# Kernel tuning notes

Measured on AMD Instinct MI355X. Metric: run time of the kernel, lower is better.

The kernel has to match this reference:

```python
import jax, jax.numpy as jnp
import numpy as np
import math

D_MODEL = 1024
N_HEAD = 16          # sub-heads per branch
N_BR = 4             # hardcoded n_branches
DH = D_MODEL // N_HEAD
H_TOT = N_BR * N_HEAD
B, T = 1, 1024
SCALE = math.pi / math.sqrt(3.0)
ATTNSCALE = DH ** -0.5


def _rope(x):
    # x: [B, H, T, D]; matches torch RoPE: even/odd split, concat halves
    t_len, d = x.shape[2], x.shape[-1]
    inv_freq = 1.0 / (10000.0 ** (jnp.arange(0, d, 2, dtype=jnp.float32) / d))
    freqs = jnp.arange(t_len, dtype=jnp.float32)[:, None] * inv_freq[None, :]  # [T, D/2]
    cos, sin = jnp.cos(freqs), jnp.sin(freqs)
    x1, x2 = x[..., 0::2], x[..., 1::2]
    return jnp.concatenate([-x2 * sin + x1 * cos, x1 * sin + x2 * cos], axis=-1)


def setup_inputs() -> dict:
    key = jax.random.key(0)
    ks = jax.random.split(key, 12)
    s = D_MODEL ** -0.5
    return {
        "X": jax.random.normal(ks[0], (B, T, D_MODEL), jnp.float32),
        "W_Q": jax.random.normal(ks[1], (D_MODEL, D_MODEL * N_BR), jnp.float32) * s,
        "b_Q": jax.random.normal(ks[2], (D_MODEL * N_BR,), jnp.float32) * 0.02,
        "W_K": jax.random.normal(ks[3], (D_MODEL, D_MODEL), jnp.float32) * s,
        "b_K": jax.random.normal(ks[4], (D_MODEL,), jnp.float32) * 0.02,
        "W_V": jax.random.normal(ks[5], (D_MODEL, D_MODEL), jnp.float32) * s,
        "b_V": jax.random.normal(ks[6], (D_MODEL,), jnp.float32) * 0.02,
        "sink_scalars": jax.random.uniform(ks[7], (H_TOT,), jnp.float32, 0.0, 0.1),
        "v_nulls": jax.random.normal(ks[8], (N_BR, D_MODEL), jnp.float32) * 0.02,
        "W_O": jax.random.normal(ks[9], (N_BR, D_MODEL, D_MODEL), jnp.float32) * s,
        "W_O_bias": jax.random.normal(ks[10], (N_BR, D_MODEL), jnp.float32) * 0.02,
    }


def reference(X, W_Q, b_Q, W_K, b_K, W_V, b_V, sink_scalars, v_nulls, W_O, W_O_bias):
    Bv, Tv, C = X.shape
    # projections -> [B, H, T, Dh]
    q = (X @ W_Q + b_Q).reshape(Bv, Tv, H_TOT, DH).transpose(0, 2, 1, 3)
    k_base = (X @ W_K + b_K).reshape(Bv, Tv, N_HEAD, DH).transpose(0, 2, 1, 3)
    v_base = (X @ W_V + b_V).reshape(Bv, Tv, N_HEAD, DH).transpose(0, 2, 1, 3)
    k = jnp.tile(k_base, (1, N_BR, 1, 1))
    v = jnp.tile(v_base, (1, N_BR, 1, 1))
    q, k = _rope(q), _rope(k)

    scores = jnp.einsum("bhtd,bhsd->bhts", q, k) * ATTNSCALE
    key_self = jnp.clip(jnp.sum(k * k, axis=-1), 1e-6, None)      # [B,H,S]
    w = jax.nn.softplus(scores / jnp.sqrt(key_self)[:, :, None, :])
    causal = jnp.tril(jnp.ones((Tv, Tv), bool))                    # [T,S]
    w = jnp.where(causal, w, 0.0)
    w = w * jax.nn.sigmoid(SCALE * w)
    sinks = sink_scalars.reshape(1, H_TOT, 1, 1)
    w = jnp.where(w < sinks, 0.0, w)
    # concat-with-sink renormalization, expressed without the concat
    total = jnp.sum(w, axis=-1, keepdims=True) + sinks + 1e-6      # [B,H,T,1]
    probs_tokens = w / total
    probs_sink = sinks / total                                     # [B,H,T,1]

    out = jnp.einsum("bhts,bhsd->bhtd", probs_tokens, v)
    v_null = v_nulls.reshape(H_TOT, DH)[None, :, None, :]          # [1,H,1,Dh]
    out = out + probs_sink * v_null

    context = out.reshape(Bv, N_BR, N_HEAD, Tv, DH).transpose(0, 1, 3, 2, 4)
    context = context.reshape(Bv, N_BR, Tv, C)
    y = jnp.einsum("bntc,ncd->bntd", context, W_O) + W_O_bias[None, :, None, :]
    return y.mean(axis=1)
```

## Files before the change

### kernel.cpp

```cpp
#include <hip/hip_runtime.h>
#include <math.h>

typedef __attribute__((ext_vector_type(4))) float  f32x4;
typedef __attribute__((ext_vector_type(8))) short  bf16x8;
typedef __attribute__((ext_vector_type(4))) short  s16x4;

#define SQUISH_U 1.8137993642342178f
#define LN2F     0.69314718055994531f

__device__ __forceinline__ float b2f(short u) {
    union { float f; unsigned b; } v; v.b = ((unsigned)(unsigned short)u) << 16; return v.f;
}
__device__ __forceinline__ short f2b(float f) {
    union { float f; unsigned b; } v; v.f = f;
    unsigned r = (v.b + 0x7FFFu + ((v.b >> 16) & 1u)) >> 16;
    return (short)r;
}
__device__ __forceinline__ unsigned cvt_pk_bf16(float lo, float hi) {
    unsigned r;
    asm("v_cvt_pk_bf16_f32 %0, %1, %2" : "=v"(r) : "v"(lo), "v"(hi));
    return r;
}
__device__ __forceinline__ void gll16(const void* g, void* l) {
    __builtin_amdgcn_global_load_lds((const __attribute__((address_space(1))) void*)g,
                                     (__attribute__((address_space(3))) void*)l, 16, 0, 0);
}
__device__ __forceinline__ void gll4(const void* g, void* l) {
    __builtin_amdgcn_global_load_lds((const __attribute__((address_space(1))) void*)g,
                                     (__attribute__((address_space(3))) void*)l, 4, 0, 0);
}

__device__ __forceinline__ void do_transpose(const float* __restrict__ src, int R, int C,
                                             short* __restrict__ dst, float scale,
                                             int c0, int r0, float (*tile)[65], int tid) {
    #pragma unroll
    for (int it = 0; it < 4; ++it) {
        int lin = it * 256 + tid;
        int r = lin >> 4, c4 = lin & 15;
        f32x4 v = *(const f32x4*)(src + (size_t)(r0 + r) * C + c0 + c4 * 4);
        #pragma unroll
        for (int k = 0; k < 4; ++k) tile[r][c4 * 4 + k] = v[k];
    }
    __syncthreads();
    #pragma unroll
    for (int it = 0; it < 4; ++it) {
        int lin = it * 256 + tid;
        int c = lin >> 4, rq = lin & 15;
        s16x4 o;
        #pragma unroll
        for (int k = 0; k < 4; ++k) o[k] = f2b(tile[rq * 4 + k][c] * scale);
        *(s16x4*)(dst + (size_t)(c0 + c) * R + r0 + rq * 4) = o;
    }
}

__global__ __launch_bounds__(256) void prep_kernel(
    const float* __restrict__ X, const float* __restrict__ W_Q, const float* __restrict__ W_K,
    const float* __restrict__ W_V, const float* __restrict__ W_O,
    const float* __restrict__ bQ, const float* __restrict__ bK, const float* __restrict__ bV,
    const float* __restrict__ bO,
    short* __restrict__ Xb, short* __restrict__ WbT, short* __restrict__ WoT,
    float* __restrict__ biasQKV, float* __restrict__ out) {
    __shared__ float tile[64][65];
    const int bid = blockIdx.x, tid = threadIdx.x;
    if (bid < 256) {
        int i = (bid * 256 + tid) * 16;
        #pragma unroll
        for (int k = 0; k < 4; ++k) {
            f32x4 v = *(const f32x4*)(X + i + k * 4);
            s16x4 o;
            o.x = f2b(v.x); o.y = f2b(v.y); o.z = f2b(v.z); o.w = f2b(v.w);
            *(s16x4*)(Xb + i + k * 4) = o;
        }
    } else if (bid < 1280) {
        int b2 = bid - 256;
        do_transpose(W_Q, 1024, 4096, WbT, 1.f, (b2 & 63) * 64, (b2 >> 6) * 64, tile, tid);
    } else if (bid < 1536) {
        int b2 = bid - 1280;
        do_transpose(W_K, 1024, 1024, WbT + 4096 * 1024, 1.f, (b2 & 15) * 64, (b2 >> 4) * 64, tile, tid);
    } else if (bid < 1792) {
        int b2 = bid - 1536;
        do_transpose(W_V, 1024, 1024, WbT + 5120 * 1024, 1.f, (b2 & 15) * 64, (b2 >> 4) * 64, tile, tid);
    } else if (bid < 2816) {
        int b2 = bid - 1792;
        do_transpose(W_O, 4096, 1024, WoT, 0.25f, (b2 & 15) * 64, (b2 >> 4) * 64, tile, tid);
    } else if (bid < 2840) {
        int i = (bid - 2816) * 256 + tid;
        if (i < 4096)      biasQKV[i] = bQ[i];
        else if (i < 5120) biasQKV[i] = bK[i - 4096];
        else               biasQKV[i] = bV[i - 5120];
    } else {
        int i = ((bid - 2840) * 256 + tid) * 4;
        f32x4 v;
        #pragma unroll
        for (int k = 0; k < 4; ++k) {
            int c = (i + k) & 1023;
            v[k] = 0.25f * (bO[c] + bO[1024 + c] + bO[2048 + c] + bO[3072 + c]);
        }
        *(f32x4*)(out + i) = v;
    }
}

#define GSTAGE_64x128(k0_, b_) do {                                            \
    _Pragma("unroll")                                                          \
    for (int it = 0; it < 2; ++it) {                                           \
        int lin0 = it * 256 + wave * 64;                                       \
        int lin = lin0 + lane;                                                 \
        int r = lin >> 3, c = (lin & 7) ^ (r & 7);                             \
        gll16(A + (size_t)(m0 + r) * K + (k0_) + c * 8, (char*)lA[b_] + lin0 * 16); \
    }                                                                          \
    _Pragma("unroll")                                                          \
    for (int it = 0; it < 4; ++it) {                                           \
        int lin0 = it * 256 + wave * 64;                                       \
        int lin = lin0 + lane;                                                 \
        int r = lin >> 3, c = (lin & 7) ^ (r & 7);                             \
        gll16(BT + (size_t)(n0 + r) * K + (k0_) + c * 8, (char*)lB[b_] + lin0 * 16); \
    } } while (0)

#define GEMM_CORE_64x128(kbeg_, kend_)                                         \
    GSTAGE_64x128(kbeg_, 0);                                                   \
    int cur = 0;                                                               \
    for (int k0 = (kbeg_); k0 < (kend_); k0 += 64) {                           \
        if (k0 + 64 < (kend_)) {                                               \
            GSTAGE_64x128(k0 + 64, cur ^ 1);                                   \
            asm volatile("s_waitcnt vmcnt(6) lgkmcnt(0)" ::: "memory");        \
        } else {                                                               \
            asm volatile("s_waitcnt vmcnt(0) lgkmcnt(0)" ::: "memory");        \
        }                                                                      \
        __builtin_amdgcn_s_barrier();                                          \
        _Pragma("unroll")                                                      \
        for (int kk = 0; kk < 2; ++kk) {                                       \
            bf16x8 af[2], bf_[4];                                              \
            _Pragma("unroll")                                                  \
            for (int m = 0; m < 2; ++m) {                                      \
                int row = wr * 32 + m * 16 + l15;                              \
                int ch = (kk * 4 + l4) ^ (row & 7);                            \
                af[m] = *(const bf16x8*)&lA[cur][row][ch << 3];                \
            }                                                                  \
            _Pragma("unroll")                                                  \
            for (int n = 0; n < 4; ++n) {                                      \
                int row = wc * 64 + n * 16 + l15;                              \
                int ch = (kk * 4 + l4) ^ (row & 7);                            \
                bf_[n] = *(const bf16x8*)&lB[cur][row][ch << 3];               \
            }                                                                  \
            _Pragma("unroll")                                                  \
            for (int m = 0; m < 2; ++m)                                        \
                _Pragma("unroll")                                              \
                for (int n = 0; n < 4; ++n)                                    \
                    acc[m][n] = __builtin_amdgcn_mfma_f32_16x16x32_bf16(af[m], bf_[n], acc[m][n], 0, 0, 0); \
        }                                                                      \
        asm volatile("" ::: "memory");                                         \
        __builtin_amdgcn_s_barrier();                                          \
        cur ^= 1;                                                              \
    }

__global__ __launch_bounds__(256, 3) void gemm_qkvf_kernel(
    const short* __restrict__ A, const short* __restrict__ BT,
    const float* __restrict__ bias, short* __restrict__ QKVb,
    short* __restrict__ Vtb, float* __restrict__ ksr,
    int M, int N, int K) {
    __shared__ short lA[2][64][64];
    __shared__ short lB[2][128][64];
    const int tid = threadIdx.x;
    const int lane = tid & 63, wave = tid >> 6;
    const int l15 = lane & 15, l4 = lane >> 4;
    const int wr = wave >> 1, wc = wave & 1;
    const int n0 = blockIdx.x * 128, m0 = blockIdx.y * 64;

    f32x4 acc[2][4];
    const f32x4 fz = {0.f, 0.f, 0.f, 0.f};
    #pragma unroll
    for (int m = 0; m < 2; ++m)
        #pragma unroll
        for (int n = 0; n < 4; ++n) acc[m][n] = fz;

    GEMM_CORE_64x128(0, K);

    const int head = blockIdx.x * 2 + wc;
    float bn[4];
    #pragma unroll
    for (int n = 0; n < 4; ++n) bn[n] = bias[head * 64 + n * 16 + l15];
    #pragma unroll
    for (int m = 0; m < 2; ++m)
        #pragma unroll
        for (int n = 0; n < 4; ++n)
            #pragma unroll
            for (int r = 0; r < 4; ++r) acc[m][n][r] += bn[n];

    if (head < 80) {
        const float invf0 = __builtin_exp2f(-(float)l15 * 0.41524101186092033f);
        const float invf1 = invf0 * 0.01f;
        const int p1 = (2 * l15) & 15, p2 = (2 * l15 + 1) & 15;
        #pragma unroll
        for (int m = 0; m < 2; ++m) {
            int tb = m0 + wr * 32 + m * 16 + l4 * 4;
            float x1lo[4], x2lo[4], x1hi[4], x2hi[4];
            #pragma unroll
            for (int r = 0; r < 4; ++r) {
                float a0 = __shfl(acc[m][0][r], p1, 16), b0 = __shfl(acc[m][1][r], p1, 16);
                float a1 = __shfl(acc[m][0][r], p2, 16), b1 = __shfl(acc[m][1][r], p2, 16);
                x1lo[r] = (l15 < 8) ? a0 : b0;
                x2lo[r] = (l15 < 8) ? a1 : b1;
                float c0 = __shfl(acc[m][2][r], p1, 16), d0 = __shfl(acc[m][3][r], p1, 16);
                float c1 = __shfl(acc[m][2][r], p2, 16), d1 = __shfl(acc[m][3][r], p2, 16);
                x1hi[r] = (l15 < 8) ? c0 : d0;
                x2hi[r] = (l15 < 8) ? c1 : d1;
            }
            #pragma unroll
            for (int r = 0; r < 4; ++r) {
                float tf = (float)(tb + r);
                float f0 = tf * invf0, f1 = tf * invf1;
                float s0 = __sinf(f0), c0 = __cosf(f0);
                float s1 = __sinf(f1), c1 = __cosf(f1);
                acc[m][0][r] = x1lo[r] * c0 - x2lo[r] * s0;
                acc[m][2][r] = x1lo[r] * s0 + x2lo[r] * c0;
                acc[m][1][r] = x1hi[r] * c1 - x2hi[r] * s1;
                acc[m][3][r] = x1hi[r] * s1 + x2hi[r] * c1;
            }
        }
    }

    if (head >= 80) {
        const int h16 = head - 80;
        #pragma unroll
        for (int m = 0; m < 2; ++m) {
            int tb = m0 + wr * 32 + m * 16 + l4 * 4;
            #pragma unroll
            for (int n = 0; n < 4; ++n) {
                s16x4 o;
                #pragma unroll
                for (int r = 0; r < 4; ++r) o[r] = f2b(acc[m][n][r]);
                *(s16x4*)(Vtb + (size_t)(h16 * 64 + n * 16 + l15) * 1024 + tb) = o;
            }
        }
    } else {
        const size_t coff = (head < 64) ? (size_t)head * 64 : (size_t)(4096 + (head - 64) * 64);
        #pragma unroll
        for (int m = 0; m < 2; ++m)
            #pragma unroll
            for (int r = 0; r < 4; ++r) {
                int row = m0 + wr * 32 + m * 16 + l4 * 4 + r;
                #pragma unroll
                for (int n = 0; n < 4; ++n)
                    QKVb[(size_t)row * 6144 + coff + n * 16 + l15] = f2b(acc[m][n][r]);
            }
        if (head >= 64) {
            const int h16 = head - 64;
            #pragma unroll
            for (int m = 0; m < 2; ++m)
                #pragma unroll
                for (int r = 0; r < 4; ++r) {
                    float ss = 0.f;
                    #pragma unroll
                    for (int n = 0; n < 4; ++n) ss += acc[m][n][r] * acc[m][n][r];
                    ss += __shfl_xor(ss, 1, 16);
                    ss += __shfl_xor(ss, 2, 16);
                    ss += __shfl_xor(ss, 4, 16);
                    ss += __shfl_xor(ss, 8, 16);
                    if (l15 == 0)
                        ksr[h16 * 1024 + m0 + wr * 32 + m * 16 + l4 * 4 + r] =
                            0.18033688011112042f * rsqrtf(fmaxf(ss, 1e-6f));
                }
        }
    }
}

__global__ __launch_bounds__(256, 3) void gemm_op_kernel(
    const short* __restrict__ A, const short* __restrict__ BT,
    float* __restrict__ out, int M, int N, int K, int KSLICE) {
    __shared__ short lA[2][64][64];
    __shared__ short lB[2][128][64];
    const int tid = threadIdx.x;
    const int lane = tid & 63, wave = tid >> 6;
    const int l15 = lane & 15, l4 = lane >> 4;
    const int wr = wave >> 1, wc = wave & 1;
    const int n0 = blockIdx.x * 128, m0 = blockIdx.y * 64;
    const int kbeg = blockIdx.z * KSLICE, kend = kbeg + KSLICE;

    f32x4 acc[2][4];
    const f32x4 fz = {0.f, 0.f, 0.f, 0.f};
    #pragma unroll
    for (int m = 0; m < 2; ++m)
        #pragma unroll
        for (int n = 0; n < 4; ++n) acc[m][n] = fz;

    GEMM_CORE_64x128(kbeg, kend);

    #pragma unroll
    for (int m = 0; m < 2; ++m)
        #pragma unroll
        for (int n = 0; n < 4; ++n)
            #pragma unroll
            for (int r = 0; r < 4; ++r) {
                int row = m0 + wr * 32 + m * 16 + l4 * 4 + r;
                int col = n0 + wc * 64 + n * 16 + l15;
                unsafeAtomicAdd(&out[(size_t)row * N + col], acc[m][n][r]);
            }
}

__constant__ __device__ const signed char TQT[24] = {15,15,14, 7,14,13,13,12, 6,12,11,11,10, 5,10, 9, 9, 8, 4, 8, 3, 2, 1, 0};
__constant__ __device__ const signed char TKB[24] = { 0, 8, 0, 0, 8, 0, 7, 0, 0, 7, 0, 6, 0, 0, 6, 0, 5, 0, 0, 5, 0, 0, 0, 0};
__constant__ __device__ const signed char TKE[24] = { 8,16, 8, 8,15, 7,14, 7, 7,13, 6,12, 6, 6,11, 5,10, 5, 5, 9, 4, 3, 2, 1};

__global__ __launch_bounds__(256, 6) void attn_kernel(
    const short* __restrict__ QKVb, const short* __restrict__ Vtb,
    const float* __restrict__ ksr, const float* __restrict__ sinks,
    const float* __restrict__ vnulls, short* __restrict__ Ob,
    float* __restrict__ Of0, float* __restrict__ Of1,
    float* __restrict__ tot0, float* __restrict__ tot1) {
    __shared__ short lK[64][64];
    __shared__ short lV[64][64];
    __shared__ float lks[64];
    __shared__ float lvn[64];
    __shared__ short lP[4][16][64];

    const int tid = threadIdx.x;
    const int lane = tid & 63, wave = tid >> 6;
    const int l15 = lane & 15, l4 = lane >> 4;
    const int h = blockIdx.x;
    const int slot = blockIdx.y;
    const int qt = TQT[slot], kb = TKB[slot], ke = TKE[slot];
    const bool single = (kb == 0) && (ke == qt + 1);
    const int h16 = h & 15;
    const int t0 = qt * 64;
    const float sink = sinks[h];
    if (tid < 64) lvn[tid] = vnulls[h * 64 + tid];

    const int q_abs = t0 + wave * 16 + l15;
    bf16x8 aq[2];
    #pragma unroll
    for (int kk = 0; kk < 2; ++kk)
        aq[kk] = *(const bf16x8*)(QKVb + (size_t)q_abs * 6144 + h * 64 + kk * 32 + l4 * 8);

    const f32x4 fz = {0.f, 0.f, 0.f, 0.f};
    f32x4 acc_o[4];
    #pragma unroll
    for (int n = 0; n < 4; ++n) acc_o[n] = fz;
    float tot = 0.f;

#define ASTAGE(s0_) do {                                                              \
    int lin0 = wave * 64;                                                             \
    int lin = lin0 + lane;                                                            \
    int r = lin >> 3, c = (lin & 7) ^ (r & 7);                                        \
    gll16(QKVb + (size_t)((s0_) + r) * 6144 + 4096 + h16 * 64 + c * 8, (char*)lK + lin0 * 16); \
    gll16(Vtb + (size_t)(h16 * 64 + r) * 1024 + (s0_) + c * 8,         (char*)lV + lin0 * 16); \
    lin0 += 256; lin = lin0 + lane; r = lin >> 3; c = (lin & 7) ^ (r & 7);            \
    gll16(QKVb + (size_t)((s0_) + r) * 6144 + 4096 + h16 * 64 + c * 8, (char*)lK + lin0 * 16); \
    gll16(Vtb + (size_t)(h16 * 64 + r) * 1024 + (s0_) + c * 8,         (char*)lV + lin0 * 16); \
    gll4(ksr + h16 * 1024 + (s0_) + lane, (char*)lks);                                \
} while (0)

    for (int kt = kb; kt < ke; ++kt) {
        int s0 = kt * 64;
        __syncthreads();
        ASTAGE(s0);
        asm volatile("s_waitcnt vmcnt(0)" ::: "memory");
        __syncthreads();

        f32x4 accs[4];
        #pragma unroll
        for (int n = 0; n < 4; ++n) accs[n] = fz;
        #pragma unroll
        for (int kk = 0; kk < 2; ++kk) {
            bf16x8 bk[4];
            #pragma unroll
            for (int n = 0; n < 4; ++n) {
                int row = n * 16 + l15;
                int ch = (kk * 4 + l4) ^ (row & 7);
                bk[n] = *(const bf16x8*)&lK[row][ch << 3];
            }
            #pragma unroll
            for (int n = 0; n < 4; ++n)
                accs[n] = __builtin_amdgcn_mfma_f32_16x16x32_bf16(bk[n], aq[kk], accs[n], 0, 0, 0);
        }

        #pragma unroll
        for (int n = 0; n < 4; ++n) {
            f32x4 ksv = *(const f32x4*)&lks[n * 16 + l4 * 4];
            float w4[4];
            #pragma unroll
            for (int r = 0; r < 4; ++r) {
                int k_abs = s0 + n * 16 + l4 * 4 + r;
                float zz = accs[n][r] * ksv[r];
                float t = __builtin_amdgcn_exp2f(zz);
                float u = __builtin_amdgcn_logf(1.f + t);
                u = (k_abs <= q_abs) ? u : 0.f;
                float g = __builtin_amdgcn_rcpf(1.f + __builtin_amdgcn_exp2f(-SQUISH_U * u));
                float w = LN2F * u * g;
                w = (w >= sink) ? w : 0.f;
                tot += w;
                w4[r] = w;
            }
            unsigned pa = cvt_pk_bf16(w4[0], w4[1]);
            unsigned pb = cvt_pk_bf16(w4[2], w4[3]);
            int ch = (2 * n + (l4 >> 1)) ^ (l15 & 7);
            uint2 val; val.x = pa; val.y = pb;
            *(uint2*)&lP[wave][l15][ch * 8 + (l4 & 1) * 4] = val;
        }

        #pragma unroll
        for (int kk = 0; kk < 2; ++kk) {
            bf16x8 ap = *(const bf16x8*)&lP[wave][l15][((kk * 4 + l4) ^ (l15 & 7)) << 3];
            bf16x8 bv[4];
            #pragma unroll
            for (int n = 0; n < 4; ++n) {
                int row = n * 16 + l15;
                int ch = (kk * 4 + l4) ^ (row & 7);
                bv[n] = *(const bf16x8*)&lV[row][ch << 3];
            }
            #pragma unroll
            for (int n = 0; n < 4; ++n)
                acc_o[n] = __builtin_amdgcn_mfma_f32_16x16x32_bf16(ap, bv[n], acc_o[n], 0, 0, 0);
        }
    }
#undef ASTAGE

    tot += __shfl_xor(tot, 16, 64);
    tot += __shfl_xor(tot, 32, 64);

    if (single) {
        float tq[4];
        #pragma unroll
        for (int r = 0; r < 4; ++r) tq[r] = __shfl(tot, l4 * 4 + r, 64);
        #pragma unroll
        for (int r = 0; r < 4; ++r) {
            float inv = __builtin_amdgcn_rcpf(tq[r] + sink + 1e-6f);
            int trow = t0 + wave * 16 + l4 * 4 + r;
            #pragma unroll
            for (int n = 0; n < 4; ++n) {
                int d = n * 16 + l15;
                float val = (acc_o[n][r] + sink * lvn[d]) * inv;
                Ob[(size_t)trow * 4096 + h * 64 + d] = f2b(val);
            }
        }
    } else {
        float* Op = (kb == 0) ? Of0 : Of1;
        float* tp = (kb == 0) ? tot0 : tot1;
        if (lane < 16) tp[h * 512 + (t0 - 512) + wave * 16 + l15] = tot;
        #pragma unroll
        for (int r = 0; r < 4; ++r) {
            int pr = h * 512 + (t0 - 512) + wave * 16 + l4 * 4 + r;
            #pragma unroll
            for (int n = 0; n < 4; ++n)
                Op[(size_t)pr * 64 + n * 16 + l15] = acc_o[n][r];
        }
    }
}

__global__ __launch_bounds__(256) void norm_kernel(
    const float* __restrict__ Of0, const float* __restrict__ Of1,
    const float* __restrict__ tot0, const float* __restrict__ tot1,
    const float* __restrict__ sinks, const float* __restrict__ vnulls,
    short* __restrict__ Ob) {
    int gid = blockIdx.x * 256 + threadIdx.x;
    int i4 = gid * 4;
    int row = i4 >> 6;
    int d0 = i4 & 63;
    int h = row >> 9;
    int t = 512 + (row & 511);
    float sink = sinks[h];
    float inv = __builtin_amdgcn_rcpf(tot0[row] + tot1[row] + sink + 1e-6f);
    f32x4 a = *(const f32x4*)(Of0 + i4);
    f32x4 b = *(const f32x4*)(Of1 + i4);
    s16x4 rs;
    #pragma unroll
    for (int k = 0; k < 4; ++k)
        rs[k] = f2b((a[k] + b[k] + sink * vnulls[h * 64 + d0 + k]) * inv);
    *(s16x4*)(Ob + (size_t)t * 4096 + h * 64 + d0) = rs;
}

extern "C" void kernel_launch(void* const* d_in, const int* in_sizes, int n_in,
                              void* d_out, int out_size, void* d_ws, size_t ws_size,
                              hipStream_t stream) {
    const float* X        = (const float*)d_in[0];
    const float* W_Q      = (const float*)d_in[1];
    const float* b_Q      = (const float*)d_in[2];
    const float* W_K      = (const float*)d_in[3];
    const float* b_K      = (const float*)d_in[4];
    const float* W_V      = (const float*)d_in[5];
    const float* b_V      = (const float*)d_in[6];
    const float* sinks    = (const float*)d_in[7];
    const float* v_nulls  = (const float*)d_in[8];
    const float* W_O      = (const float*)d_in[9];
    const float* W_O_bias = (const float*)d_in[10];
    float* out = (float*)d_out;
    char* ws = (char*)d_ws;

    short* Xb        = (short*)(ws + 0);
    short* WbT       = (short*)(ws + 2097152);
    short* WoT       = (short*)(ws + 14680064);
    short* QKVb      = (short*)(ws + 23068672);
    short* Vtb       = (short*)(ws + 35651584);
    short* Ob        = (short*)(ws + 37748736);
    float* ksr       = (float*)(ws + 46137344);
    float* biasQKV   = (float*)(ws + 46202880);
    float* Of0       = (float*)(ws + 50331648);
    float* Of1       = (float*)(ws + 58720256);
    float* tot0      = (float*)(ws + 67108864);
    float* tot1      = (float*)(ws + 67239936);

    prep_kernel<<<3864, 256, 0, stream>>>(X, W_Q, W_K, W_V, W_O, b_Q, b_K, b_V, W_O_bias,
                                          Xb, WbT, WoT, biasQKV, out);
    gemm_qkvf_kernel<<<dim3(48, 16), 256, 0, stream>>>(Xb, WbT, biasQKV, QKVb, Vtb, ksr,
                                                       1024, 6144, 1024);
    attn_kernel<<<dim3(64, 24), 256, 0, stream>>>(QKVb, Vtb, ksr, sinks, v_nulls, Ob,
                                                  Of0, Of1, tot0, tot1);
    norm_kernel<<<2048, 256, 0, stream>>>(Of0, Of1, tot0, tot1, sinks, v_nulls, Ob);
    gemm_op_kernel<<<dim3(8, 16, 4), 256, 0, stream>>>(Ob, WoT, out, 1024, 1024, 4096, 1024);
}
```

Baseline: 184.4 us.

## Use 128x128 32x32 MFMA tiles in output GEMM and prefetch K/V in attention

The output-projection GEMM moves from 64x128 tiles with 16x16 MFMAs to 128x128 tiles with 32x32x16 MFMAs. It double-buffers its LDS staging and changes the split-K layout to 8 slices of 512, keeping the grid at 512 blocks. The attention kernel now prefetches the next K/V tile into registers while computing the current one, then writes it to LDS, instead of load-wait-compute. This aims to raise MFMA efficiency and hide global load latency, at the cost of more LDS and registers, lower occupancy, and more atomic adds from the extra K slices.

```diff
diff --git a/kernel.cpp b/kernel.cpp
--- a/kernel.cpp
+++ b/kernel.cpp
@@ -1,9 +1,10 @@
 #include <hip/hip_runtime.h>
 #include <math.h>
 
-typedef __attribute__((ext_vector_type(4))) float  f32x4;
-typedef __attribute__((ext_vector_type(8))) short  bf16x8;
-typedef __attribute__((ext_vector_type(4))) short  s16x4;
+typedef __attribute__((ext_vector_type(4)))  float f32x4;
+typedef __attribute__((ext_vector_type(16))) float f32x16;
+typedef __attribute__((ext_vector_type(8)))  short bf16x8;
+typedef __attribute__((ext_vector_type(4)))  short s16x4;
 
 #define SQUISH_U 1.8137993642342178f
 #define LN2F     0.69314718055994531f
@@ -264,36 +265,98 @@
     }
 }
 
-__global__ __launch_bounds__(256, 3) void gemm_op_kernel(
+__global__ __launch_bounds__(256, 2) void gemm_op_kernel(
     const short* __restrict__ A, const short* __restrict__ BT,
     float* __restrict__ out, int M, int N, int K, int KSLICE) {
-    __shared__ short lA[2][64][64];
+    __shared__ short lA[2][128][64];
     __shared__ short lB[2][128][64];
     const int tid = threadIdx.x;
     const int lane = tid & 63, wave = tid >> 6;
-    const int l15 = lane & 15, l4 = lane >> 4;
+    const int l31 = lane & 31, l5 = lane >> 5;
     const int wr = wave >> 1, wc = wave & 1;
-    const int n0 = blockIdx.x * 128, m0 = blockIdx.y * 64;
+    const int n0 = blockIdx.x * 128, m0 = blockIdx.y * 128;
     const int kbeg = blockIdx.z * KSLICE, kend = kbeg + KSLICE;
 
-    f32x4 acc[2][4];
-    const f32x4 fz = {0.f, 0.f, 0.f, 0.f};
+    f32x16 acc[2][2];
     #pragma unroll
     for (int m = 0; m < 2; ++m)
         #pragma unroll
-        for (int n = 0; n < 4; ++n) acc[m][n] = fz;
-
-    GEMM_CORE_64x128(kbeg, kend);
-
+        for (int n = 0; n < 2; ++n)
+            #pragma unroll
+            for (int g = 0; g < 16; ++g) acc[m][n][g] = 0.f;
+
+#define GSTAGE_128(k0_, b_) do {                                               \
+    _Pragma("unroll")                                                          \
+    for (int it = 0; it < 4; ++it) {                                           \
+        int lin0 = it * 256 + wave * 64;                                       \
+        int lin = lin0 + lane;                                                 \
+        int r = lin >> 3, c = (lin & 7) ^ (r & 7);                             \
+        gll16(A  + (size_t)(m0 + r) * K + (k0_) + c * 8, (char*)lA[b_] + lin0 * 16); \
+        gll16(BT + (size_t)(n0 + r) * K + (k0_) + c * 8, (char*)lB[b_] + lin0 * 16); \
+    } } while (0)
+
+    GSTAGE_128(kbeg, 0);
+    int cur = 0;
+    for (int k0 = kbeg; k0 < kend; k0 += 64) {
+        if (k0 + 64 < kend) {
+            GSTAGE_128(k0 + 64, cur ^ 1);
+            asm volatile("s_waitcnt vmcnt(8) lgkmcnt(0)" ::: "memory");
+        } else {
+            asm volatile("s_waitcnt vmcnt(0) lgkmcnt(0)" ::: "memory");
+        }
+        __builtin_amdgcn_s_barrier();
+        #pragma unroll
+        for (int kk = 0; kk < 2; ++kk) {
+            bf16x8 af[2], bf_[2];
+            #pragma unroll
+            for (int m = 0; m < 2; ++m) {
+                int row = wr * 64 + m * 32 + l31;
+                int ch = (kk * 2 + l5) ^ (row & 7);
+                af[m] = *(const bf16x8*)&lA[cur][row][ch << 3];
+            }
+            #pragma unroll
+            for (int n = 0; n < 2; ++n) {
+                int row = wc * 64 + n * 32 + l31;
+                int ch = (kk * 2 + l5) ^ (row & 7);
+                bf_[n] = *(const bf16x8*)&lB[cur][row][ch << 3];
+            }
+            #pragma unroll
+            for (int m = 0; m < 2; ++m)
+                #pragma unroll
+                for (int n = 0; n < 2; ++n)
+                    acc[m][n] = __builtin_amdgcn_mfma_f32_32x32x16_bf16(af[m], bf_[n], acc[m][n], 0, 0, 0);
+            #pragma unroll
+            for (int m = 0; m < 2; ++m) {
+                int row = wr * 64 + m * 32 + l31;
+                int ch = (4 + kk * 2 + l5) ^ (row & 7);
+                af[m] = *(const bf16x8*)&lA[cur][row][ch << 3];
+            }
+            #pragma unroll
+            for (int n = 0; n < 2; ++n) {
+                int row = wc * 64 + n * 32 + l31;
+                int ch = (4 + kk * 2 + l5) ^ (row & 7);
+                bf_[n] = *(const bf16x8*)&lB[cur][row][ch << 3];
+            }
+            #pragma unroll
+            for (int m = 0; m < 2; ++m)
+                #pragma unroll
+                for (int n = 0; n < 2; ++n)
+                    acc[m][n] = __builtin_amdgcn_mfma_f32_32x32x16_bf16(af[m], bf_[n], acc[m][n], 0, 0, 0);
+        }
+        asm volatile("" ::: "memory");
+        __builtin_amdgcn_s_barrier();
+        cur ^= 1;
+    }
+#undef GSTAGE_128
     #pragma unroll
     for (int m = 0; m < 2; ++m)
         #pragma unroll
-        for (int n = 0; n < 4; ++n)
-            #pragma unroll
-            for (int r = 0; r < 4; ++r) {
-                int row = m0 + wr * 32 + m * 16 + l4 * 4 + r;
-                int col = n0 + wc * 64 + n * 16 + l15;
-                unsafeAtomicAdd(&out[(size_t)row * N + col], acc[m][n][r]);
+        for (int n = 0; n < 2; ++n)
+            #pragma unroll
+            for (int g = 0; g < 16; ++g) {
+                int row = m0 + wr * 64 + m * 32 + (g & 3) + 8 * (g >> 2) + 4 * l5;
+                int col = n0 + wc * 64 + n * 32 + l31;
+                unsafeAtomicAdd(&out[(size_t)row * N + col], acc[m][n][g]);
             }
 }
 
@@ -337,24 +400,34 @@
     for (int n = 0; n < 4; ++n) acc_o[n] = fz;
     float tot = 0.f;
 
-#define ASTAGE(s0_) do {                                                              \
-    int lin0 = wave * 64;                                                             \
-    int lin = lin0 + lane;                                                            \
-    int r = lin >> 3, c = (lin & 7) ^ (r & 7);                                        \
-    gll16(QKVb + (size_t)((s0_) + r) * 6144 + 4096 + h16 * 64 + c * 8, (char*)lK + lin0 * 16); \
-    gll16(Vtb + (size_t)(h16 * 64 + r) * 1024 + (s0_) + c * 8,         (char*)lV + lin0 * 16); \
-    lin0 += 256; lin = lin0 + lane; r = lin >> 3; c = (lin & 7) ^ (r & 7);            \
-    gll16(QKVb + (size_t)((s0_) + r) * 6144 + 4096 + h16 * 64 + c * 8, (char*)lK + lin0 * 16); \
-    gll16(Vtb + (size_t)(h16 * 64 + r) * 1024 + (s0_) + c * 8,         (char*)lV + lin0 * 16); \
-    gll4(ksr + h16 * 1024 + (s0_) + lane, (char*)lks);                                \
-} while (0)
+    const int linA = wave * 64 + lane;
+    const int rA = linA >> 3, cA = (linA & 7) ^ (rA & 7);
+    const int linB = linA + 256;
+    const int rB = linB >> 3, cB = (linB & 7) ^ (rB & 7);
+
+    {
+        int s0 = kb * 64;
+        gll16(QKVb + (size_t)(s0 + rA) * 6144 + 4096 + h16 * 64 + cA * 8, (char*)lK + (linA - lane) * 16);
+        gll16(Vtb + (size_t)(h16 * 64 + rA) * 1024 + s0 + cA * 8,         (char*)lV + (linA - lane) * 16);
+        gll16(QKVb + (size_t)(s0 + rB) * 6144 + 4096 + h16 * 64 + cB * 8, (char*)lK + (linB - lane - 256) * 16 + 4096);
+        gll16(Vtb + (size_t)(h16 * 64 + rB) * 1024 + s0 + cB * 8,         (char*)lV + (linB - lane - 256) * 16 + 4096);
+        gll4(ksr + h16 * 1024 + s0 + lane, (char*)lks);
+        asm volatile("s_waitcnt vmcnt(0)" ::: "memory");
+        __syncthreads();
+    }
 
     for (int kt = kb; kt < ke; ++kt) {
         int s0 = kt * 64;
-        __syncthreads();
-        ASTAGE(s0);
-        asm volatile("s_waitcnt vmcnt(0)" ::: "memory");
-        __syncthreads();
+        const bool pf = (kt + 1 < ke);
+        uint4 rk0, rv0, rk1, rv1; float rks;
+        if (pf) {
+            int s1 = s0 + 64;
+            rk0 = *(const uint4*)(QKVb + (size_t)(s1 + rA) * 6144 + 4096 + h16 * 64 + cA * 8);
+            rv0 = *(const uint4*)(Vtb + (size_t)(h16 * 64 + rA) * 1024 + s1 + cA * 8);
+            rk1 = *(const uint4*)(QKVb + (size_t)(s1 + rB) * 6144 + 4096 + h16 * 64 + cB * 8);
+            rv1 = *(const uint4*)(Vtb + (size_t)(h16 * 64 + rB) * 1024 + s1 + cB * 8);
+            rks = ksr[h16 * 1024 + s1 + lane];
+        }
 
         f32x4 accs[4];
         #pragma unroll
@@ -411,8 +484,17 @@
             for (int n = 0; n < 4; ++n)
                 acc_o[n] = __builtin_amdgcn_mfma_f32_16x16x32_bf16(ap, bv[n], acc_o[n], 0, 0, 0);
         }
-    }
-#undef ASTAGE
+
+        __syncthreads();
+        if (pf) {
+            *(uint4*)((char*)lK + (size_t)linA * 16) = rk0;
+            *(uint4*)((char*)lV + (size_t)linA * 16) = rv0;
+            *(uint4*)((char*)lK + (size_t)linB * 16) = rk1;
+            *(uint4*)((char*)lV + (size_t)linB * 16) = rv1;
+            lks[lane] = rks;
+        }
+        __syncthreads();
+    }
 
     tot += __shfl_xor(tot, 16, 64);
     tot += __shfl_xor(tot, 32, 64);
@@ -505,5 +587,5 @@
     attn_kernel<<<dim3(64, 24), 256, 0, stream>>>(QKVb, Vtb, ksr, sinks, v_nulls, Ob,
                                                   Of0, Of1, tot0, tot1);
     norm_kernel<<<2048, 256, 0, stream>>>(Of0, Of1, tot0, tot1, sinks, v_nulls, Ob);
-    gemm_op_kernel<<<dim3(8, 16, 4), 256, 0, stream>>>(Ob, WoT, out, 1024, 1024, 4096, 1024);
-}
+    gemm_op_kernel<<<dim3(8, 8, 8), 256, 0, stream>>>(Ob, WoT, out, 1024, 1024, 4096, 512);
+}
```

Result: slower. 217.8 us (+18.1%).

## Process two heads sharing the same K/V per attention block

Applied to the files above, without the earlier changes.

Each attention block now handles two query heads (pid and pid+32) that map to the same shared K/V sub-head. The block loads each K/V tile once and reuses it for both heads, halving the grid to 32x24 and halving K/V staging traffic. Register pressure roughly doubles for accumulators, so launch bounds drop from 6 to 4 waves per SIMD. Fewer blocks (768) means less parallelism on a 256-CU device.

```diff
diff --git a/kernel.cpp b/kernel.cpp
--- a/kernel.cpp
+++ b/kernel.cpp
@@ -301,7 +301,7 @@
 __constant__ __device__ const signed char TKB[24] = { 0, 8, 0, 0, 8, 0, 7, 0, 0, 7, 0, 6, 0, 0, 6, 0, 5, 0, 0, 5, 0, 0, 0, 0};
 __constant__ __device__ const signed char TKE[24] = { 8,16, 8, 8,15, 7,14, 7, 7,13, 6,12, 6, 6,11, 5,10, 5, 5, 9, 4, 3, 2, 1};
 
-__global__ __launch_bounds__(256, 6) void attn_kernel(
+__global__ __launch_bounds__(256, 4) void attn_kernel(
     const short* __restrict__ QKVb, const short* __restrict__ Vtb,
     const float* __restrict__ ksr, const float* __restrict__ sinks,
     const float* __restrict__ vnulls, short* __restrict__ Ob,
@@ -310,32 +310,38 @@
     __shared__ short lK[64][64];
     __shared__ short lV[64][64];
     __shared__ float lks[64];
-    __shared__ float lvn[64];
+    __shared__ float lvn[2][64];
     __shared__ short lP[4][16][64];
 
     const int tid = threadIdx.x;
     const int lane = tid & 63, wave = tid >> 6;
     const int l15 = lane & 15, l4 = lane >> 4;
-    const int h = blockIdx.x;
+    const int pid = blockIdx.x;
     const int slot = blockIdx.y;
     const int qt = TQT[slot], kb = TKB[slot], ke = TKE[slot];
     const bool single = (kb == 0) && (ke == qt + 1);
-    const int h16 = h & 15;
+    const int h16 = pid & 15;
     const int t0 = qt * 64;
-    const float sink = sinks[h];
-    if (tid < 64) lvn[tid] = vnulls[h * 64 + tid];
+    const int hh0 = pid, hh1 = pid + 32;
+    const float sk0 = sinks[hh0], sk1 = sinks[hh1];
+    if (tid < 64)       lvn[0][tid] = vnulls[hh0 * 64 + tid];
+    else if (tid < 128) lvn[1][tid - 64] = vnulls[hh1 * 64 + (tid - 64)];
 
     const int q_abs = t0 + wave * 16 + l15;
-    bf16x8 aq[2];
-    #pragma unroll
-    for (int kk = 0; kk < 2; ++kk)
-        aq[kk] = *(const bf16x8*)(QKVb + (size_t)q_abs * 6144 + h * 64 + kk * 32 + l4 * 8);
+    bf16x8 aq[2][2];
+    #pragma unroll
+    for (int kk = 0; kk < 2; ++kk) {
+        aq[0][kk] = *(const bf16x8*)(QKVb + (size_t)q_abs * 6144 + hh0 * 64 + kk * 32 + l4 * 8);
+        aq[1][kk] = *(const bf16x8*)(QKVb + (size_t)q_abs * 6144 + hh1 * 64 + kk * 32 + l4 * 8);
+    }
 
     const f32x4 fz = {0.f, 0.f, 0.f, 0.f};
-    f32x4 acc_o[4];
-    #pragma unroll
-    for (int n = 0; n < 4; ++n) acc_o[n] = fz;
-    float tot = 0.f;
+    f32x4 acc_o[2][4];
+    float tot[2] = {0.f, 0.f};
+    #pragma unroll
+    for (int b = 0; b < 2; ++b)
+        #pragma unroll
+        for (int n = 0; n < 4; ++n) acc_o[b][n] = fz;
 
 #define ASTAGE(s0_) do {                                                              \
     int lin0 = wave * 64;                                                             \
@@ -356,92 +362,102 @@
         asm volatile("s_waitcnt vmcnt(0)" ::: "memory");
         __syncthreads();
 
-        f32x4 accs[4];
-        #pragma unroll
-        for (int n = 0; n < 4; ++n) accs[n] = fz;
-        #pragma unroll
-        for (int kk = 0; kk < 2; ++kk) {
-            bf16x8 bk[4];
+        #pragma unroll
+        for (int b = 0; b < 2; ++b) {
+            const float sink = b ? sk1 : sk0;
+            f32x4 accs[4];
+            #pragma unroll
+            for (int n = 0; n < 4; ++n) accs[n] = fz;
+            #pragma unroll
+            for (int kk = 0; kk < 2; ++kk) {
+                bf16x8 bk[4];
+                #pragma unroll
+                for (int n = 0; n < 4; ++n) {
+                    int row = n * 16 + l15;
+                    int ch = (kk * 4 + l4) ^ (row & 7);
+                    bk[n] = *(const bf16x8*)&lK[row][ch << 3];
+                }
+                #pragma unroll
+                for (int n = 0; n < 4; ++n)
+                    accs[n] = __builtin_amdgcn_mfma_f32_16x16x32_bf16(bk[n], aq[b][kk], accs[n], 0, 0, 0);
+            }
+
             #pragma unroll
             for (int n = 0; n < 4; ++n) {
-                int row = n * 16 + l15;
-                int ch = (kk * 4 + l4) ^ (row & 7);
-                bk[n] = *(const bf16x8*)&lK[row][ch << 3];
-            }
-            #pragma unroll
-            for (int n = 0; n < 4; ++n)
-                accs[n] = __builtin_amdgcn_mfma_f32_16x16x32_bf16(bk[n], aq[kk], accs[n], 0, 0, 0);
-        }
-
-        #pragma unroll
-        for (int n = 0; n < 4; ++n) {
-            f32x4 ksv = *(const f32x4*)&lks[n * 16 + l4 * 4];
-            float w4[4];
+                f32x4 ksv = *(const f32x4*)&lks[n * 16 + l4 * 4];
+                float w4[4];
+                #pragma unroll
+                for (int r = 0; r < 4; ++r) {
+                    int k_abs = s0 + n * 16 + l4 * 4 + r;
+                    float zz = accs[n][r] * ksv[r];
+                    float t = __builtin_amdgcn_exp2f(zz);
+                    float u = __builtin_amdgcn_logf(1.f + t);
+                    u = (k_abs <= q_abs) ? u : 0.f;
+                    float g = __builtin_amdgcn_rcpf(1.f + __builtin_amdgcn_exp2f(-SQUISH_U * u));
+                    float w = LN2F * u * g;
+                    w = (w >= sink) ? w : 0.f;
+                    tot[b] += w;
+                    w4[r] = w;
+                }
+                unsigned pa = cvt_pk_bf16(w4[0], w4[1]);
+                unsigned pb = cvt_pk_bf16(w4[2], w4[3]);
+                int ch = (2 * n + (l4 >> 1)) ^ (l15 & 7);
+                uint2 val; val.x = pa; val.y = pb;
+                *(uint2*)&lP[wave][l15][ch * 8 + (l4 & 1) * 4] = val;
+            }
+
+            #pragma unroll
+            for (int kk = 0; kk < 2; ++kk) {
+                bf16x8 ap = *(const bf16x8*)&lP[wave][l15][((kk * 4 + l4) ^ (l15 & 7)) << 3];
+                bf16x8 bv[4];
+                #pragma unroll
+                for (int n = 0; n < 4; ++n) {
+                    int row = n * 16 + l15;
+                    int ch = (kk * 4 + l4) ^ (row & 7);
+                    bv[n] = *(const bf16x8*)&lV[row][ch << 3];
+                }
+                #pragma unroll
+                for (int n = 0; n < 4; ++n)
+                    acc_o[b][n] = __builtin_amdgcn_mfma_f32_16x16x32_bf16(ap, bv[n], acc_o[b][n], 0, 0, 0);
+            }
+        }
+    }
+#undef ASTAGE
+
+    #pragma unroll
+    for (int b = 0; b < 2; ++b) {
+        const int hh = b ? hh1 : hh0;
+        const float sink = b ? sk1 : sk0;
+        float t = tot[b];
+        t += __shfl_xor(t, 16, 64);
+        t += __shfl_xor(t, 32, 64);
+
+        if (single) {
+            float tq[4];
+            #pragma unroll
+            for (int r = 0; r < 4; ++r) tq[r] = __shfl(t, l4 * 4 + r, 64);
             #pragma unroll
             for (int r = 0; r < 4; ++r) {
-                int k_abs = s0 + n * 16 + l4 * 4 + r;
-                float zz = accs[n][r] * ksv[r];
-                float t = __builtin_amdgcn_exp2f(zz);
-                float u = __builtin_amdgcn_logf(1.f + t);
-                u = (k_abs <= q_abs) ? u : 0.f;
-                float g = __builtin_amdgcn_rcpf(1.f + __builtin_amdgcn_exp2f(-SQUISH_U * u));
-                float w = LN2F * u * g;
-                w = (w >= sink) ? w : 0.f;
-                tot += w;
-                w4[r] = w;
-            }
-            unsigned pa = cvt_pk_bf16(w4[0], w4[1]);
-            unsigned pb = cvt_pk_bf16(w4[2], w4[3]);
-            int ch = (2 * n + (l4 >> 1)) ^ (l15 & 7);
-            uint2 val; val.x = pa; val.y = pb;
-            *(uint2*)&lP[wave][l15][ch * 8 + (l4 & 1) * 4] = val;
-        }
-
-        #pragma unroll
-        for (int kk = 0; kk < 2; ++kk) {
-            bf16x8 ap = *(const bf16x8*)&lP[wave][l15][((kk * 4 + l4) ^ (l15 & 7)) << 3];
-            bf16x8 bv[4];
-            #pragma unroll
-            for (int n = 0; n < 4; ++n) {
-                int row = n * 16 + l15;
-                int ch = (kk * 4 + l4) ^ (row & 7);
-                bv[n] = *(const bf16x8*)&lV[row][ch << 3];
-            }
-            #pragma unroll
-            for (int n = 0; n < 4; ++n)
-                acc_o[n] = __builtin_amdgcn_mfma_f32_16x16x32_bf16(ap, bv[n], acc_o[n], 0, 0, 0);
-        }
-    }
-#undef ASTAGE
-
-    tot += __shfl_xor(tot, 16, 64);
-    tot += __shfl_xor(tot, 32, 64);
-
-    if (single) {
-        float tq[4];
-        #pragma unroll
-        for (int r = 0; r < 4; ++r) tq[r] = __shfl(tot, l4 * 4 + r, 64);
-        #pragma unroll
-        for (int r = 0; r < 4; ++r) {
-            float inv = __builtin_amdgcn_rcpf(tq[r] + sink + 1e-6f);
-            int trow = t0 + wave * 16 + l4 * 4 + r;
-            #pragma unroll
-            for (int n = 0; n < 4; ++n) {
-                int d = n * 16 + l15;
-                float val = (acc_o[n][r] + sink * lvn[d]) * inv;
-                Ob[(size_t)trow * 4096 + h * 64 + d] = f2b(val);
-            }
-        }
-    } else {
-        float* Op = (kb == 0) ? Of0 : Of1;
-        float* tp = (kb == 0) ? tot0 : tot1;
-        if (lane < 16) tp[h * 512 + (t0 - 512) + wave * 16 + l15] = tot;
-        #pragma unroll
-        for (int r = 0; r < 4; ++r) {
-            int pr = h * 512 + (t0 - 512) + wave * 16 + l4 * 4 + r;
-            #pragma unroll
-            for (int n = 0; n < 4; ++n)
-                Op[(size_t)pr * 64 + n * 16 + l15] = acc_o[n][r];
+                float inv = __builtin_amdgcn_rcpf(tq[r] + sink + 1e-6f);
+                int trow = t0 + wave * 16 + l4 * 4 + r;
+                #pragma unroll
+                for (int n = 0; n < 4; ++n) {
+                    int d = n * 16 + l15;
+                    float val = (acc_o[b][n][r] + sink * lvn[b][d]) * inv;
+                    Ob[(size_t)trow * 4096 + hh * 64 + d] = f2b(val);
+                }
+            }
+        } else {
+            float* Op = (kb == 0) ? Of0 : Of1;
+            float* tp = (kb == 0) ? tot0 : tot1;
+            if (lane < 16) tp[hh * 512 + (t0 - 512) + wave * 16 + l15] = t;
+            #pragma unroll
+            for (int r = 0; r < 4; ++r) {
+                int pr = hh * 512 + (t0 - 512) + wave * 16 + l4 * 4 + r;
+                #pragma unroll
+                for (int n = 0; n < 4; ++n)
+                    Op[(size_t)pr * 64 + n * 16 + l15] = acc_o[b][n][r];
+            }
         }
     }
 }
@@ -502,7 +518,7 @@
                                           Xb, WbT, WoT, biasQKV, out);
     gemm_qkvf_kernel<<<dim3(48, 16), 256, 0, stream>>>(Xb, WbT, biasQKV, QKVb, Vtb, ksr,
                                                        1024, 6144, 1024);
-    attn_kernel<<<dim3(64, 24), 256, 0, stream>>>(QKVb, Vtb, ksr, sinks, v_nulls, Ob,
+    attn_kernel<<<dim3(32, 24), 256, 0, stream>>>(QKVb, Vtb, ksr, sinks, v_nulls, Ob,
                                                   Of0, Of1, tot0, tot1);
     norm_kernel<<<2048, 256, 0, stream>>>(Of0, Of1, tot0, tot1, sinks, v_nulls, Ob);
     gemm_op_kernel<<<dim3(8, 16, 4), 256, 0, stream>>>(Ob, WoT, out, 1024, 1024, 4096, 1024);
```

New measurement: 195.3 us. 1.06x slower.
